# Kernel tuning notes

Hardware: AMD Instinct MI355X
Metric: run time of the kernel (lower is better)

Reference implementation:

```python
import jax, jax.numpy as jnp
import numpy as np

B, S, D, H = 2, 2048, 1024, 16
HD = D // H  # head_dim = 64


def setup_inputs() -> dict:
    key = jax.random.key(0)
    ks = jax.random.split(key, 9)
    sc = 1.0 / np.sqrt(D)
    return {
        "X": jax.random.normal(ks[0], (B, S, D), jnp.float32),
        "Wq": jax.random.normal(ks[1], (D, D), jnp.float32) * sc,
        "bq": jnp.zeros((D,), jnp.float32),
        "Wk": jax.random.normal(ks[2], (D, D), jnp.float32) * sc,
        "bk": jnp.zeros((D,), jnp.float32),
        "Wv": jax.random.normal(ks[3], (D, D), jnp.float32) * sc,
        "bv": jnp.zeros((D,), jnp.float32),
        "Wo": jax.random.normal(ks[4], (D, D), jnp.float32) * sc,
        "bo": jnp.zeros((D,), jnp.float32),
    }


def reference(X, Wq, bq, Wk, bk, Wv, bv, Wo, bo):
    b, s, d = X.shape
    q = (X @ Wq + bq).reshape(b, s, H, HD).transpose(0, 2, 1, 3)  # [B,H,S,HD]
    k = (X @ Wk + bk).reshape(b, s, H, HD).transpose(0, 2, 1, 3)
    v = (X @ Wv + bv).reshape(b, s, H, HD).transpose(0, 2, 1, 3)
    score = jnp.einsum("bhqd,bhkd->bhqk", q, k) / jnp.sqrt(jnp.float32(HD))
    causal = jnp.tril(jnp.ones((s, s), bool))  # [S,S]
    score = jnp.where(causal[None, None], score, -jnp.inf)
    attn = jax.nn.softmax(score, axis=-1)
    out = jnp.einsum("bhqk,bhkd->bhqd", attn, v)  # [B,H,S,HD]
    out = out.transpose(0, 2, 1, 3).reshape(b, s, d)
    return out @ Wo + bo
```

## Files before the change

kernel.cpp:

```cpp
#include <hip/hip_runtime.h>
#include <hip/hip_bf16.h>
#include <math.h>

#define B_SZ 2
#define S_SZ 2048
#define D_SZ 1024
#define H_SZ 16
#define HD_SZ 64
constexpr int M_ROWS = B_SZ * S_SZ;

typedef __bf16 bf16x8 __attribute__((ext_vector_type(8)));
typedef __bf16 bf16x4 __attribute__((ext_vector_type(4)));
typedef float f32x4 __attribute__((ext_vector_type(4)));

#define GLOAD_LDS16(gsrc, ldst)                                              \
  __builtin_amdgcn_global_load_lds(                                          \
      (const __attribute__((address_space(1))) void*)(gsrc),                 \
      (__attribute__((address_space(3))) void*)(ldst), 16, 0, 0)

__global__ __launch_bounds__(256) void cvt_bf16(const float* __restrict__ in,
                                                __bf16* __restrict__ out,
                                                int n8) {
  const int i = blockIdx.x * 256 + threadIdx.x;
  if (i >= n8) return;
  const float4 a = *reinterpret_cast<const float4*>(&in[i * 8]);
  const float4 b = *reinterpret_cast<const float4*>(&in[i * 8 + 4]);
  bf16x8 o;
  o[0] = (__bf16)a.x; o[1] = (__bf16)a.y; o[2] = (__bf16)a.z; o[3] = (__bf16)a.w;
  o[4] = (__bf16)b.x; o[5] = (__bf16)b.y; o[6] = (__bf16)b.z; o[7] = (__bf16)b.w;
  *reinterpret_cast<bf16x8*>(&out[i * 8]) = o;
}

__global__ __launch_bounds__(256) void cvt_w_t_all(const float* __restrict__ W0,
                                                   const float* __restrict__ W1,
                                                   const float* __restrict__ W2,
                                                   const float* __restrict__ W3,
                                                   __bf16* __restrict__ Wt) {
  __shared__ float Ts[32][33];
  const int z = blockIdx.z;
  const float* W = z == 0 ? W0 : (z == 1 ? W1 : (z == 2 ? W2 : W3));
  __bf16* out = Wt + (size_t)z * 1024 * 1024;
  const int k0 = blockIdx.x * 32, n0 = blockIdx.y * 32;
  const int tr = threadIdx.x >> 3;
  const int tc = (threadIdx.x & 7) * 4;
  const float4 v = *reinterpret_cast<const float4*>(&W[(size_t)(k0 + tr) * 1024 + n0 + tc]);
  Ts[tr][tc + 0] = v.x;
  Ts[tr][tc + 1] = v.y;
  Ts[tr][tc + 2] = v.z;
  Ts[tr][tc + 3] = v.w;
  __syncthreads();
  bf16x4 o;
#pragma unroll
  for (int j = 0; j < 4; ++j) o[j] = (__bf16)Ts[tc + j][tr];
  *reinterpret_cast<bf16x4*>(&out[(size_t)(n0 + tr) * 1024 + k0 + tc]) = o;
}

__global__ __launch_bounds__(256) void transpose_v(const __bf16* __restrict__ V,
                                                   __bf16* __restrict__ Vt) {
  constexpr int TST = 66;
  __shared__ __bf16 T[64 * TST];
  const int bh = blockIdx.y;
  const int s0 = blockIdx.x * 64;
  const size_t base = (size_t)bh * S_SZ * HD_SZ;
  const int tid = threadIdx.x;
  for (int i = tid; i < 512; i += 256) {
    const int r = i >> 3, c = (i & 7) * 8;
    *reinterpret_cast<bf16x8*>(&T[r * TST + c]) =
        *reinterpret_cast<const bf16x8*>(&V[base + (size_t)(s0 + r) * 64 + c]);
  }
  __syncthreads();
  const size_t obase = (size_t)bh * HD_SZ * S_SZ;
  for (int i = tid; i < 512; i += 256) {
    const int d = i >> 3, c = (i & 7) * 8;
    bf16x8 o;
#pragma unroll
    for (int j = 0; j < 8; ++j) o[j] = T[(c + j) * TST + d];
    *reinterpret_cast<bf16x8*>(&Vt[obase + (size_t)d * S_SZ + s0 + c]) = o;
  }
}

template <int MODE>
__global__ __launch_bounds__(256) void gemm_mfma(
    const __bf16* __restrict__ Ab, const __bf16* __restrict__ Bt,
    const float* __restrict__ bias0, const float* __restrict__ bias1,
    const float* __restrict__ bias2, float* __restrict__ C0,
    __bf16* __restrict__ Q0, __bf16* __restrict__ K0, __bf16* __restrict__ V0,
    int M, int N, int K) {
  __shared__ __bf16 As[2][128 * 32];
  __shared__ __bf16 Bs[2][128 * 32];

  const int tid = threadIdx.x;
  const int lane = tid & 63;
  const int w = tid >> 6;
  const int lr = lane & 15, lg = lane >> 4;
  const int wr = w >> 1, wc = w & 1;
  const int bm = blockIdx.x * 128;
  const int bn = blockIdx.y * 128;

  const int r0 = tid >> 2, c0 = (tid & 3) * 8;
  const int r1 = (tid + 256) >> 2, c1 = ((tid + 256) & 3) * 8;
  const __bf16* aS0 = &Ab[(size_t)(bm + r0) * K + c0];
  const __bf16* aS1 = &Ab[(size_t)(bm + r1) * K + c1];
  const __bf16* bS0 = &Bt[(size_t)(bn + r0) * K + c0];
  const __bf16* bS1 = &Bt[(size_t)(bn + r1) * K + c1];

  f32x4 acc[4][4] = {};

  auto STAGE = [&](int buf) {
    GLOAD_LDS16(aS0, &As[buf][w * 512]);
    GLOAD_LDS16(aS1, &As[buf][2048 + w * 512]);
    GLOAD_LDS16(bS0, &Bs[buf][w * 512]);
    GLOAD_LDS16(bS1, &Bs[buf][2048 + w * 512]);
    aS0 += 32; aS1 += 32; bS0 += 32; bS1 += 32;
  };

  STAGE(0);
  asm volatile("s_waitcnt vmcnt(0)" ::: "memory");
  __builtin_amdgcn_s_barrier();
  __builtin_amdgcn_sched_barrier(0);
  int cur = 0;

  for (int k0 = 0; k0 < K; k0 += 32) {
    const bool has_next = (k0 + 32 < K);
    if (has_next) STAGE(cur ^ 1);
    if (k0) {
      if (has_next)
        asm volatile("s_waitcnt vmcnt(4)" ::: "memory");
      else
        asm volatile("s_waitcnt vmcnt(0)" ::: "memory");
      __builtin_amdgcn_s_barrier();
      __builtin_amdgcn_sched_barrier(0);
    }

    bf16x8 af[4], bfr[4];
#pragma unroll
    for (int i = 0; i < 4; ++i)
      af[i] = *reinterpret_cast<const bf16x8*>(&As[cur][(wr * 64 + i * 16 + lr) * 32 + lg * 8]);
#pragma unroll
    for (int j = 0; j < 4; ++j)
      bfr[j] = *reinterpret_cast<const bf16x8*>(&Bs[cur][(wc * 64 + j * 16 + lr) * 32 + lg * 8]);
    __builtin_amdgcn_s_setprio(1);
#pragma unroll
    for (int i = 0; i < 4; ++i)
#pragma unroll
      for (int j = 0; j < 4; ++j)
        acc[i][j] = __builtin_amdgcn_mfma_f32_16x16x32_bf16(af[i], bfr[j], acc[i][j], 0, 0, 0);
    __builtin_amdgcn_s_setprio(0);
    __builtin_amdgcn_sched_barrier(0);
    __builtin_amdgcn_s_barrier();
    cur ^= 1;
  }

  if (MODE == 0) {
#pragma unroll
    for (int j = 0; j < 4; ++j) {
      const int n = bn + wc * 64 + j * 16 + lr;
      const float bs = bias0[n];
#pragma unroll
      for (int i = 0; i < 4; ++i) {
        const int mrow = bm + wr * 64 + i * 16 + lg * 4;
#pragma unroll
        for (int r = 0; r < 4; ++r)
          C0[(size_t)(mrow + r) * N + n] = acc[i][j][r] + bs;
      }
    }
  } else {
    const int which = bn >> 10;
    __bf16* dst = which == 0 ? Q0 : (which == 1 ? K0 : V0);
    const float* bp = which == 0 ? bias0 : (which == 1 ? bias1 : bias2);
    const float scale = which == 0 ? 0.18033688011112042f : 1.0f;
#pragma unroll
    for (int j = 0; j < 4; ++j) {
      const int nn = (bn & 1023) + wc * 64 + j * 16 + lr;
      const int hh = nn >> 6, hd = nn & 63;
      const float bs = bp[nn];
#pragma unroll
      for (int i = 0; i < 4; ++i) {
        const int mrow = bm + wr * 64 + i * 16 + lg * 4;
#pragma unroll
        for (int r = 0; r < 4; ++r) {
          const int m = mrow + r;
          const int bb = m >> 11, ss = m & (S_SZ - 1);
          dst[(((size_t)(bb * H_SZ + hh)) * S_SZ + ss) * HD_SZ + hd] =
              (__bf16)((acc[i][j][r] + bs) * scale);
        }
      }
    }
  }
}

__global__ __launch_bounds__(256) void attn_mfma(const __bf16* __restrict__ Q,
                                                 const __bf16* __restrict__ Kg,
                                                 const __bf16* __restrict__ Vtg,
                                                 __bf16* __restrict__ Aout) {
  constexpr int PST = 40;
  __shared__ __bf16 Ks[2][64 * 64];
  __shared__ __bf16 Vts[2][64 * 64];
  __shared__ __bf16 Ps[4][16 * PST];

  const int tid = threadIdx.x;
  const int lane = tid & 63;
  const int w = tid >> 6;
  const int lr = lane & 15;
  const int lg = lane >> 4;

  const int flat = blockIdx.x;
  const int qb = 31 - (flat >> 5);
  const int hb = flat & 31;
  const int h = hb >> 1, b = hb & 1;
  const size_t base = (size_t)(b * H_SZ + h) * S_SZ * HD_SZ;
  const int q0 = qb * 64 + w * 16;

  bf16x8 aq[2];
#pragma unroll
  for (int hh = 0; hh < 2; ++hh)
    aq[hh] = *reinterpret_cast<const bf16x8*>(
        &Q[base + (size_t)(q0 + lr) * 64 + hh * 32 + lg * 8]);

  const int srow = lane >> 3;
  const int schunk = (lane & 7) ^ srow;

  bf16x8 ones8;
#pragma unroll
  for (int j = 0; j < 8; ++j) ones8[j] = (__bf16)1.0f;

  f32x4 oacc[4] = {};
  f32x4 oacc_l = {};

  const int ntiles = qb + 1;

  const int rbA = w * 16, rbB = w * 16 + 8;
  const __bf16* kS0 = &Kg[base + (size_t)(rbA + srow) * 64 + schunk * 8];
  const __bf16* kS1 = &Kg[base + (size_t)(rbB + srow) * 64 + schunk * 8];
  const __bf16* vS0 = &Vtg[base + (size_t)(rbA + srow) * S_SZ + schunk * 8];
  const __bf16* vS1 = &Vtg[base + (size_t)(rbB + srow) * S_SZ + schunk * 8];

  auto ISSUE = [&](int buf) {
    GLOAD_LDS16(kS0, &Ks[buf][rbA * 64]);
    GLOAD_LDS16(kS1, &Ks[buf][rbB * 64]);
    GLOAD_LDS16(vS0, &Vts[buf][rbA * 64]);
    GLOAD_LDS16(vS1, &Vts[buf][rbB * 64]);
  };

  ISSUE(0);
  asm volatile("s_waitcnt vmcnt(0)" ::: "memory");
  __builtin_amdgcn_s_barrier();
  __builtin_amdgcn_sched_barrier(0);
  int cur = 0;

  for (int t0 = 0; t0 < ntiles; ++t0) {
    const bool has_next = (t0 + 1 < ntiles);
    if (has_next) {
      kS0 += 64 * 64; kS1 += 64 * 64;
      vS0 += 64;      vS1 += 64;
      ISSUE(cur ^ 1);
    }
    if (t0) {
      if (has_next)
        asm volatile("s_waitcnt vmcnt(4)" ::: "memory");
      else
        asm volatile("s_waitcnt vmcnt(0)" ::: "memory");
      __builtin_amdgcn_s_barrier();
      __builtin_amdgcn_sched_barrier(0);
    }

    f32x4 s[4];
    __builtin_amdgcn_s_setprio(1);
#pragma unroll
    for (int t = 0; t < 4; ++t) {
      const int row = t * 16 + lr;
      const bf16x8 k0f = *reinterpret_cast<const bf16x8*>(
          &Ks[cur][row * 64 + ((lg ^ (lr & 7)) * 8)]);
      const bf16x8 k1f = *reinterpret_cast<const bf16x8*>(
          &Ks[cur][row * 64 + (((4 | lg) ^ (lr & 7)) * 8)]);
      f32x4 z = (f32x4){0.f, 0.f, 0.f, 0.f};
      z = __builtin_amdgcn_mfma_f32_16x16x32_bf16(aq[0], k0f, z, 0, 0, 0);
      z = __builtin_amdgcn_mfma_f32_16x16x32_bf16(aq[1], k1f, z, 0, 0, 0);
      s[t] = z;
    }
    __builtin_amdgcn_s_setprio(0);

    if (t0 == qb) {
#pragma unroll
      for (int t = 0; t < 4; ++t) {
        const int key = t0 * 64 + t * 16 + lr;
#pragma unroll
        for (int r = 0; r < 4; ++r) {
          const int qrow = q0 + lg * 4 + r;
          if (key > qrow) s[t][r] = -INFINITY;
        }
      }
    }

#pragma unroll
    for (int t = 0; t < 4; ++t)
#pragma unroll
      for (int r = 0; r < 4; ++r)
        s[t][r] = __builtin_amdgcn_exp2f(s[t][r]);

    __bf16* const psw = &Ps[w][0];
#pragma unroll
    for (int kh = 0; kh < 2; ++kh) {
#pragma unroll
      for (int t2 = 0; t2 < 2; ++t2)
#pragma unroll
        for (int r = 0; r < 4; ++r)
          psw[(lg * 4 + r) * PST + t2 * 16 + lr] = (__bf16)s[kh * 2 + t2][r];
      asm volatile("s_waitcnt lgkmcnt(0)" ::: "memory");
      __builtin_amdgcn_sched_barrier(0);
      const bf16x8 pa = *reinterpret_cast<const bf16x8*>(&psw[lr * PST + lg * 8]);
      __builtin_amdgcn_s_setprio(1);
#pragma unroll
      for (int dc = 0; dc < 4; ++dc) {
        const int row = dc * 16 + lr;
        const bf16x8 vf = *reinterpret_cast<const bf16x8*>(
            &Vts[cur][row * 64 + (((kh * 4 + lg) ^ (lr & 7)) * 8)]);
        oacc[dc] = __builtin_amdgcn_mfma_f32_16x16x32_bf16(pa, vf, oacc[dc], 0, 0, 0);
      }
      oacc_l = __builtin_amdgcn_mfma_f32_16x16x32_bf16(pa, ones8, oacc_l, 0, 0, 0);
      __builtin_amdgcn_s_setprio(0);
      __builtin_amdgcn_sched_barrier(0);
    }

    __builtin_amdgcn_sched_barrier(0);
    __builtin_amdgcn_s_barrier();
    cur ^= 1;
  }

#pragma unroll
  for (int r = 0; r < 4; ++r) {
    const float inv = 1.f / oacc_l[r];
    const int qg = q0 + lg * 4 + r;
#pragma unroll
    for (int dc = 0; dc < 4; ++dc)
      Aout[(size_t)(b * S_SZ + qg) * D_SZ + h * 64 + dc * 16 + lr] =
          (__bf16)(oacc[dc][r] * inv);
  }
}

extern "C" void kernel_launch(void* const* d_in, const int* in_sizes, int n_in,
                              void* d_out, int out_size, void* d_ws,
                              size_t ws_size, hipStream_t stream) {
  const float* X = (const float*)d_in[0];
  const float* Wq = (const float*)d_in[1];
  const float* bq = (const float*)d_in[2];
  const float* Wk = (const float*)d_in[3];
  const float* bk = (const float*)d_in[4];
  const float* Wv = (const float*)d_in[5];
  const float* bv = (const float*)d_in[6];
  const float* Wo = (const float*)d_in[7];
  const float* bo = (const float*)d_in[8];
  float* out = (float*)d_out;

  const size_t elems = (size_t)M_ROWS * D_SZ;
  const size_t welems = (size_t)D_SZ * D_SZ;
  __bf16* Xb = (__bf16*)d_ws;
  __bf16* Wt = Xb + elems;
  __bf16* Q = Wt + 4 * welems;
  __bf16* K = Q + elems;
  __bf16* V = K + elems;
  __bf16* Vt = V + elems;
  __bf16* Ahb = Vt + elems;

  cvt_bf16<<<(int)(elems / 8 / 256), 256, 0, stream>>>(X, Xb, (int)(elems / 8));
  cvt_w_t_all<<<dim3(32, 32, 4), 256, 0, stream>>>(Wq, Wk, Wv, Wo, Wt);

  gemm_mfma<1><<<dim3(M_ROWS / 128, 3072 / 128), 256, 0, stream>>>(
      Xb, Wt, bq, bk, bv, nullptr, Q, K, V, M_ROWS, 3072, D_SZ);

  transpose_v<<<dim3(32, 32), 256, 0, stream>>>(V, Vt);

  attn_mfma<<<dim3(1024), 256, 0, stream>>>(Q, K, Vt, Ahb);

  gemm_mfma<0><<<dim3(M_ROWS / 128, D_SZ / 128), 256, 0, stream>>>(
      Ahb, Wt + 3 * welems, bo, nullptr, nullptr, out, nullptr, nullptr,
      nullptr, M_ROWS, D_SZ, D_SZ);
}
```

Before: 116.0 us.

## Use 128-query attention blocks and narrower output-projection GEMM tiles

The attention kernel now processes 128 query rows per block, 32 per wave in two row groups. Each K/V tile loaded into LDS is reused across twice as many queries, and the grid is halved with a reordered schedule that pairs heavy and light blocks. Waves whose query rows lie entirely before a key tile skip that tile's compute. The output projection GEMM uses 128x64 tiles to double its block count for better occupancy, at the cost of less reuse per block and more registers and LDS per attention wave.

```diff
diff --git a/kernel.cpp b/kernel.cpp
--- a/kernel.cpp
+++ b/kernel.cpp
@@ -79,15 +79,16 @@
   }
 }
 
-template <int MODE>
+template <int MODE, int BN>
 __global__ __launch_bounds__(256) void gemm_mfma(
     const __bf16* __restrict__ Ab, const __bf16* __restrict__ Bt,
     const float* __restrict__ bias0, const float* __restrict__ bias1,
     const float* __restrict__ bias2, float* __restrict__ C0,
     __bf16* __restrict__ Q0, __bf16* __restrict__ K0, __bf16* __restrict__ V0,
     int M, int N, int K) {
+  constexpr int NJ = BN / 32;
   __shared__ __bf16 As[2][128 * 32];
-  __shared__ __bf16 Bs[2][128 * 32];
+  __shared__ __bf16 Bs[2][BN * 32];
 
   const int tid = threadIdx.x;
   const int lane = tid & 63;
@@ -95,7 +96,7 @@
   const int lr = lane & 15, lg = lane >> 4;
   const int wr = w >> 1, wc = w & 1;
   const int bm = blockIdx.x * 128;
-  const int bn = blockIdx.y * 128;
+  const int bn = blockIdx.y * BN;
 
   const int r0 = tid >> 2, c0 = (tid & 3) * 8;
   const int r1 = (tid + 256) >> 2, c1 = ((tid + 256) & 3) * 8;
@@ -104,14 +105,15 @@
   const __bf16* bS0 = &Bt[(size_t)(bn + r0) * K + c0];
   const __bf16* bS1 = &Bt[(size_t)(bn + r1) * K + c1];
 
-  f32x4 acc[4][4] = {};
+  f32x4 acc[4][NJ] = {};
 
   auto STAGE = [&](int buf) {
     GLOAD_LDS16(aS0, &As[buf][w * 512]);
     GLOAD_LDS16(aS1, &As[buf][2048 + w * 512]);
     GLOAD_LDS16(bS0, &Bs[buf][w * 512]);
-    GLOAD_LDS16(bS1, &Bs[buf][2048 + w * 512]);
-    aS0 += 32; aS1 += 32; bS0 += 32; bS1 += 32;
+    if constexpr (BN == 128) GLOAD_LDS16(bS1, &Bs[buf][2048 + w * 512]);
+    aS0 += 32; aS1 += 32; bS0 += 32;
+    if constexpr (BN == 128) bS1 += 32;
   };
 
   STAGE(0);
@@ -124,26 +126,30 @@
     const bool has_next = (k0 + 32 < K);
     if (has_next) STAGE(cur ^ 1);
     if (k0) {
-      if (has_next)
-        asm volatile("s_waitcnt vmcnt(4)" ::: "memory");
-      else
+      if (has_next) {
+        if constexpr (BN == 128)
+          asm volatile("s_waitcnt vmcnt(4)" ::: "memory");
+        else
+          asm volatile("s_waitcnt vmcnt(3)" ::: "memory");
+      } else {
         asm volatile("s_waitcnt vmcnt(0)" ::: "memory");
+      }
       __builtin_amdgcn_s_barrier();
       __builtin_amdgcn_sched_barrier(0);
     }
 
-    bf16x8 af[4], bfr[4];
+    bf16x8 af[4], bfr[NJ];
 #pragma unroll
     for (int i = 0; i < 4; ++i)
       af[i] = *reinterpret_cast<const bf16x8*>(&As[cur][(wr * 64 + i * 16 + lr) * 32 + lg * 8]);
 #pragma unroll
-    for (int j = 0; j < 4; ++j)
-      bfr[j] = *reinterpret_cast<const bf16x8*>(&Bs[cur][(wc * 64 + j * 16 + lr) * 32 + lg * 8]);
+    for (int j = 0; j < NJ; ++j)
+      bfr[j] = *reinterpret_cast<const bf16x8*>(&Bs[cur][(wc * (BN / 2) + j * 16 + lr) * 32 + lg * 8]);
     __builtin_amdgcn_s_setprio(1);
 #pragma unroll
     for (int i = 0; i < 4; ++i)
 #pragma unroll
-      for (int j = 0; j < 4; ++j)
+      for (int j = 0; j < NJ; ++j)
         acc[i][j] = __builtin_amdgcn_mfma_f32_16x16x32_bf16(af[i], bfr[j], acc[i][j], 0, 0, 0);
     __builtin_amdgcn_s_setprio(0);
     __builtin_amdgcn_sched_barrier(0);
@@ -153,8 +159,8 @@
 
   if (MODE == 0) {
 #pragma unroll
-    for (int j = 0; j < 4; ++j) {
-      const int n = bn + wc * 64 + j * 16 + lr;
+    for (int j = 0; j < NJ; ++j) {
+      const int n = bn + wc * (BN / 2) + j * 16 + lr;
       const float bs = bias0[n];
 #pragma unroll
       for (int i = 0; i < 4; ++i) {
@@ -170,8 +176,8 @@
     const float* bp = which == 0 ? bias0 : (which == 1 ? bias1 : bias2);
     const float scale = which == 0 ? 0.18033688011112042f : 1.0f;
 #pragma unroll
-    for (int j = 0; j < 4; ++j) {
-      const int nn = (bn & 1023) + wc * 64 + j * 16 + lr;
+    for (int j = 0; j < NJ; ++j) {
+      const int nn = (bn & 1023) + wc * (BN / 2) + j * 16 + lr;
       const int hh = nn >> 6, hd = nn & 63;
       const float bs = bp[nn];
 #pragma unroll
@@ -193,10 +199,10 @@
                                                  const __bf16* __restrict__ Kg,
                                                  const __bf16* __restrict__ Vtg,
                                                  __bf16* __restrict__ Aout) {
-  constexpr int PST = 40;
+  constexpr int PST = 76;
   __shared__ __bf16 Ks[2][64 * 64];
   __shared__ __bf16 Vts[2][64 * 64];
-  __shared__ __bf16 Ps[4][16 * PST];
+  __shared__ __bf16 Ps[4][32 * PST];
 
   const int tid = threadIdx.x;
   const int lane = tid & 63;
@@ -205,17 +211,19 @@
   const int lg = lane >> 4;
 
   const int flat = blockIdx.x;
-  const int qb = 31 - (flat >> 5);
+  const int qb = (flat < 256) ? (15 - (flat >> 5)) : ((flat - 256) >> 5);
   const int hb = flat & 31;
   const int h = hb >> 1, b = hb & 1;
   const size_t base = (size_t)(b * H_SZ + h) * S_SZ * HD_SZ;
-  const int q0 = qb * 64 + w * 16;
-
-  bf16x8 aq[2];
-#pragma unroll
-  for (int hh = 0; hh < 2; ++hh)
-    aq[hh] = *reinterpret_cast<const bf16x8*>(
-        &Q[base + (size_t)(q0 + lr) * 64 + hh * 32 + lg * 8]);
+  const int q0 = qb * 128 + w * 32;
+
+  bf16x8 aq[2][2];
+#pragma unroll
+  for (int rg = 0; rg < 2; ++rg)
+#pragma unroll
+    for (int hh = 0; hh < 2; ++hh)
+      aq[rg][hh] = *reinterpret_cast<const bf16x8*>(
+          &Q[base + (size_t)(q0 + rg * 16 + lr) * 64 + hh * 32 + lg * 8]);
 
   const int srow = lane >> 3;
   const int schunk = (lane & 7) ^ srow;
@@ -224,10 +232,10 @@
 #pragma unroll
   for (int j = 0; j < 8; ++j) ones8[j] = (__bf16)1.0f;
 
-  f32x4 oacc[4] = {};
-  f32x4 oacc_l = {};
-
-  const int ntiles = qb + 1;
+  f32x4 oacc[2][4] = {};
+  f32x4 oacc_l[2] = {};
+
+  const int ntiles = 2 * qb + 2;
 
   const int rbA = w * 16, rbB = w * 16 + 8;
   const __bf16* kS0 = &Kg[base + (size_t)(rbA + srow) * 64 + schunk * 8];
@@ -264,62 +272,70 @@
       __builtin_amdgcn_sched_barrier(0);
     }
 
-    f32x4 s[4];
-    __builtin_amdgcn_s_setprio(1);
-#pragma unroll
-    for (int t = 0; t < 4; ++t) {
-      const int row = t * 16 + lr;
-      const bf16x8 k0f = *reinterpret_cast<const bf16x8*>(
-          &Ks[cur][row * 64 + ((lg ^ (lr & 7)) * 8)]);
-      const bf16x8 k1f = *reinterpret_cast<const bf16x8*>(
-          &Ks[cur][row * 64 + (((4 | lg) ^ (lr & 7)) * 8)]);
-      f32x4 z = (f32x4){0.f, 0.f, 0.f, 0.f};
-      z = __builtin_amdgcn_mfma_f32_16x16x32_bf16(aq[0], k0f, z, 0, 0, 0);
-      z = __builtin_amdgcn_mfma_f32_16x16x32_bf16(aq[1], k1f, z, 0, 0, 0);
-      s[t] = z;
-    }
-    __builtin_amdgcn_s_setprio(0);
-
-    if (t0 == qb) {
+    if (t0 * 64 <= q0 + 31) {
+      f32x4 s[2][4];
+      __builtin_amdgcn_s_setprio(1);
 #pragma unroll
       for (int t = 0; t < 4; ++t) {
-        const int key = t0 * 64 + t * 16 + lr;
-#pragma unroll
-        for (int r = 0; r < 4; ++r) {
-          const int qrow = q0 + lg * 4 + r;
-          if (key > qrow) s[t][r] = -INFINITY;
+        const int row = t * 16 + lr;
+        const bf16x8 k0f = *reinterpret_cast<const bf16x8*>(
+            &Ks[cur][row * 64 + ((lg ^ (lr & 7)) * 8)]);
+        const bf16x8 k1f = *reinterpret_cast<const bf16x8*>(
+            &Ks[cur][row * 64 + (((4 | lg) ^ (lr & 7)) * 8)]);
+#pragma unroll
+        for (int rg = 0; rg < 2; ++rg) {
+          f32x4 z = (f32x4){0.f, 0.f, 0.f, 0.f};
+          z = __builtin_amdgcn_mfma_f32_16x16x32_bf16(aq[rg][0], k0f, z, 0, 0, 0);
+          z = __builtin_amdgcn_mfma_f32_16x16x32_bf16(aq[rg][1], k1f, z, 0, 0, 0);
+          s[rg][t] = z;
         }
       }
-    }
-
-#pragma unroll
-    for (int t = 0; t < 4; ++t)
-#pragma unroll
-      for (int r = 0; r < 4; ++r)
-        s[t][r] = __builtin_amdgcn_exp2f(s[t][r]);
-
-    __bf16* const psw = &Ps[w][0];
-#pragma unroll
-    for (int kh = 0; kh < 2; ++kh) {
-#pragma unroll
-      for (int t2 = 0; t2 < 2; ++t2)
-#pragma unroll
-        for (int r = 0; r < 4; ++r)
-          psw[(lg * 4 + r) * PST + t2 * 16 + lr] = (__bf16)s[kh * 2 + t2][r];
+      __builtin_amdgcn_s_setprio(0);
+
+      if (t0 >= 2 * qb) {
+#pragma unroll
+        for (int t = 0; t < 4; ++t) {
+          const int key = t0 * 64 + t * 16 + lr;
+#pragma unroll
+          for (int rg = 0; rg < 2; ++rg)
+#pragma unroll
+            for (int r = 0; r < 4; ++r) {
+              const int qrow = q0 + rg * 16 + lg * 4 + r;
+              if (key > qrow) s[rg][t][r] = -INFINITY;
+            }
+        }
+      }
+
+#pragma unroll
+      for (int rg = 0; rg < 2; ++rg)
+#pragma unroll
+        for (int t = 0; t < 4; ++t)
+#pragma unroll
+          for (int r = 0; r < 4; ++r)
+            Ps[w][(rg * 16 + lg * 4 + r) * PST + t * 16 + lr] =
+                (__bf16)__builtin_amdgcn_exp2f(s[rg][t][r]);
       asm volatile("s_waitcnt lgkmcnt(0)" ::: "memory");
       __builtin_amdgcn_sched_barrier(0);
-      const bf16x8 pa = *reinterpret_cast<const bf16x8*>(&psw[lr * PST + lg * 8]);
+
       __builtin_amdgcn_s_setprio(1);
 #pragma unroll
-      for (int dc = 0; dc < 4; ++dc) {
-        const int row = dc * 16 + lr;
-        const bf16x8 vf = *reinterpret_cast<const bf16x8*>(
-            &Vts[cur][row * 64 + (((kh * 4 + lg) ^ (lr & 7)) * 8)]);
-        oacc[dc] = __builtin_amdgcn_mfma_f32_16x16x32_bf16(pa, vf, oacc[dc], 0, 0, 0);
-      }
-      oacc_l = __builtin_amdgcn_mfma_f32_16x16x32_bf16(pa, ones8, oacc_l, 0, 0, 0);
+      for (int kh = 0; kh < 2; ++kh) {
+        const bf16x8 pa0 = *reinterpret_cast<const bf16x8*>(
+            &Ps[w][lr * PST + kh * 32 + lg * 8]);
+        const bf16x8 pa1 = *reinterpret_cast<const bf16x8*>(
+            &Ps[w][(16 + lr) * PST + kh * 32 + lg * 8]);
+#pragma unroll
+        for (int dc = 0; dc < 4; ++dc) {
+          const int row = dc * 16 + lr;
+          const bf16x8 vf = *reinterpret_cast<const bf16x8*>(
+              &Vts[cur][row * 64 + (((kh * 4 + lg) ^ (lr & 7)) * 8)]);
+          oacc[0][dc] = __builtin_amdgcn_mfma_f32_16x16x32_bf16(pa0, vf, oacc[0][dc], 0, 0, 0);
+          oacc[1][dc] = __builtin_amdgcn_mfma_f32_16x16x32_bf16(pa1, vf, oacc[1][dc], 0, 0, 0);
+        }
+        oacc_l[0] = __builtin_amdgcn_mfma_f32_16x16x32_bf16(pa0, ones8, oacc_l[0], 0, 0, 0);
+        oacc_l[1] = __builtin_amdgcn_mfma_f32_16x16x32_bf16(pa1, ones8, oacc_l[1], 0, 0, 0);
+      }
       __builtin_amdgcn_s_setprio(0);
-      __builtin_amdgcn_sched_barrier(0);
     }
 
     __builtin_amdgcn_sched_barrier(0);
@@ -328,14 +344,16 @@
   }
 
 #pragma unroll
-  for (int r = 0; r < 4; ++r) {
-    const float inv = 1.f / oacc_l[r];
-    const int qg = q0 + lg * 4 + r;
-#pragma unroll
-    for (int dc = 0; dc < 4; ++dc)
-      Aout[(size_t)(b * S_SZ + qg) * D_SZ + h * 64 + dc * 16 + lr] =
-          (__bf16)(oacc[dc][r] * inv);
-  }
+  for (int rg = 0; rg < 2; ++rg)
+#pragma unroll
+    for (int r = 0; r < 4; ++r) {
+      const float inv = 1.f / oacc_l[rg][r];
+      const int qg = q0 + rg * 16 + lg * 4 + r;
+#pragma unroll
+      for (int dc = 0; dc < 4; ++dc)
+        Aout[(size_t)(b * S_SZ + qg) * D_SZ + h * 64 + dc * 16 + lr] =
+            (__bf16)(oacc[rg][dc][r] * inv);
+    }
 }
 
 extern "C" void kernel_launch(void* const* d_in, const int* in_sizes, int n_in,
@@ -365,14 +383,14 @@
   cvt_bf16<<<(int)(elems / 8 / 256), 256, 0, stream>>>(X, Xb, (int)(elems / 8));
   cvt_w_t_all<<<dim3(32, 32, 4), 256, 0, stream>>>(Wq, Wk, Wv, Wo, Wt);
 
-  gemm_mfma<1><<<dim3(M_ROWS / 128, 3072 / 128), 256, 0, stream>>>(
+  gemm_mfma<1, 128><<<dim3(M_ROWS / 128, 3072 / 128), 256, 0, stream>>>(
       Xb, Wt, bq, bk, bv, nullptr, Q, K, V, M_ROWS, 3072, D_SZ);
 
   transpose_v<<<dim3(32, 32), 256, 0, stream>>>(V, Vt);
 
-  attn_mfma<<<dim3(1024), 256, 0, stream>>>(Q, K, Vt, Ahb);
-
-  gemm_mfma<0><<<dim3(M_ROWS / 128, D_SZ / 128), 256, 0, stream>>>(
+  attn_mfma<<<dim3(512), 256, 0, stream>>>(Q, K, Vt, Ahb);
+
+  gemm_mfma<0, 64><<<dim3(M_ROWS / 128, D_SZ / 64), 256, 0, stream>>>(
       Ahb, Wt + 3 * welems, bo, nullptr, nullptr, out, nullptr, nullptr,
       nullptr, M_ROWS, D_SZ, D_SZ);
 }
```

Result: slower. 121.0 us (+4.3%).
